# Optimization experiments

Hardware: AMD Instinct MI355X
Metric: run time of the kernel (lower is better)

## Reference

```python
import jax, jax.numpy as jnp
import numpy as np

IMG_C = 256
GC = 32  # graph_channel; must equal graph feature dim 32 for the residual


def setup_inputs() -> dict:
    key = jax.random.key(0)
    ks = jax.random.split(key, 10)
    B, N, WH_SIDE = 8, 4096, 64
    s = lambda fan_in: 1.0 / np.sqrt(fan_in)
    return {
        "input_graph": jax.random.normal(ks[0], (B, N, GC), jnp.float32),
        "input_image": jax.random.normal(ks[1], (B, IMG_C, WH_SIDE, WH_SIDE), jnp.float32),
        # Conv1d(kernel=1) weights stored as [out, in]
        "Wq": jax.random.uniform(ks[2], (GC, 32), jnp.float32, -s(32), s(32)),
        "bq": jax.random.uniform(ks[3], (GC,), jnp.float32, -s(32), s(32)),
        "Wk": jax.random.uniform(ks[4], (GC, IMG_C), jnp.float32, -s(IMG_C), s(IMG_C)),
        "bk": jax.random.uniform(ks[5], (GC,), jnp.float32, -s(IMG_C), s(IMG_C)),
        "Wv": jax.random.uniform(ks[6], (GC, IMG_C), jnp.float32, -s(IMG_C), s(IMG_C)),
        "bv": jax.random.uniform(ks[7], (GC,), jnp.float32, -s(IMG_C), s(IMG_C)),
        "Wc": jax.random.uniform(ks[8], (GC, GC), jnp.float32, -s(GC), s(GC)),
        "bc": jax.random.uniform(ks[9], (GC,), jnp.float32, -s(GC), s(GC)),
    }


def reference(input_graph, input_image, Wq, bq, Wk, bk, Wv, bv, Wc, bc):
    B, C, W, H = input_image.shape
    img = input_image.reshape(B, C, W * H)                      # [B, C, L]
    # 1x1 conv projections == channel matmuls
    K = jnp.einsum('oc,bcl->bol', Wk, img) + bk[None, :, None]  # [B, GC, L]
    V = jnp.einsum('oc,bcl->bol', Wv, img) + bv[None, :, None]  # [B, GC, L]
    # Q: graph [B, N, 32] -> conv over channel dim -> [B, N, GC]
    Q = jnp.einsum('oc,bnc->bno', Wq, input_graph) + bq[None, None, :]
    att = jnp.einsum('bno,bol->bnl', Q, K) / jnp.sqrt(jnp.float32(GC))  # [B, N, L]
    # NOTE: original softmax is over dim=1 (the node/query axis)
    att = jax.nn.softmax(att, axis=1)
    message = jnp.einsum('bol,bnl->bon', V, att)                # [B, GC, N]
    out = input_graph.transpose(0, 2, 1) + (
        jnp.einsum('oc,bcn->bon', Wc, message) + bc[None, :, None]
    )                                                           # [B, GC, N]
    return out.transpose(0, 2, 1)                               # [B, N, GC]
```

## Files before the change

### kernel.cpp

```cpp
#include <hip/hip_runtime.h>

#define BB 8
#define NN 4096
#define LL 4096
#define CC 256

typedef short bf16x8 __attribute__((ext_vector_type(8)));
typedef _Float16 f16x8 __attribute__((ext_vector_type(8)));
typedef __fp16 hf16x2 __attribute__((ext_vector_type(2)));
typedef float f32x4 __attribute__((ext_vector_type(4)));

__device__ __forceinline__ short f2bf(float f) {
  union { float f; unsigned u; } v; v.f = f;
  unsigned r = v.u + 0x7fffu + ((v.u >> 16) & 1u);
  return (short)(r >> 16);
}
__device__ __forceinline__ bf16x8 ld8(const float* __restrict__ fp) {
  float4 a = *(const float4*)fp;
  float4 b = *(const float4*)(fp + 4);
  bf16x8 r;
  r[0] = f2bf(a.x); r[1] = f2bf(a.y); r[2] = f2bf(a.z); r[3] = f2bf(a.w);
  r[4] = f2bf(b.x); r[5] = f2bf(b.y); r[6] = f2bf(b.z); r[7] = f2bf(b.w);
  return r;
}

__global__ __launch_bounds__(256) void ka_proj(
    const float* __restrict__ graph, const float* __restrict__ img,
    const float* __restrict__ Wq, const float* __restrict__ bq,
    const float* __restrict__ Wk, const float* __restrict__ bk,
    const float* __restrict__ Wv, const float* __restrict__ bv,
    short* __restrict__ Qb, short* __restrict__ Kt, _Float16* __restrict__ Vt,
    float* __restrict__ Zbuf)
{
  const int tid = threadIdx.x;
  const int w = tid >> 6, lane = tid & 63, lo = lane & 15, q = lane >> 4;
  const int bid = blockIdx.x;
  if (bid < 512) {
    const int b = bid >> 6;
    if (tid < 64) Zbuf[(size_t)b * LL + ((bid & 63) << 6) + tid] = 0.0f;
    const int lt = ((bid & 63) << 6) + (w << 4);
    f32x4 aK0 = {0,0,0,0}, aK1 = {0,0,0,0}, aV0 = {0,0,0,0}, aV1 = {0,0,0,0};
    const float* ib = img + (size_t)b * CC * LL + lt + lo;
    #pragma unroll
    for (int cs = 0; cs < 8; ++cs) {
      const int c0 = cs * 32 + q * 8;
      bf16x8 bi;
      #pragma unroll
      for (int j = 0; j < 8; ++j) bi[j] = f2bf(ib[(size_t)(c0 + j) * LL]);
      bf16x8 wk0 = ld8(Wk + lo * CC + c0);
      bf16x8 wk1 = ld8(Wk + (lo + 16) * CC + c0);
      bf16x8 wv0 = ld8(Wv + lo * CC + c0);
      bf16x8 wv1 = ld8(Wv + (lo + 16) * CC + c0);
      aK0 = __builtin_amdgcn_mfma_f32_16x16x32_bf16(wk0, bi, aK0, 0, 0, 0);
      aK1 = __builtin_amdgcn_mfma_f32_16x16x32_bf16(wk1, bi, aK1, 0, 0, 0);
      aV0 = __builtin_amdgcn_mfma_f32_16x16x32_bf16(wv0, bi, aV0, 0, 0, 0);
      aV1 = __builtin_amdgcn_mfma_f32_16x16x32_bf16(wv1, bi, aV1, 0, 0, 0);
    }
    const float kscale = 0.2550348663f;
    const size_t row = ((size_t)b * LL + lt + lo) * 32;
    short4 s0, s1;
    s0.x = f2bf((aK0[0] + bk[q * 4 + 0]) * kscale);
    s0.y = f2bf((aK0[1] + bk[q * 4 + 1]) * kscale);
    s0.z = f2bf((aK0[2] + bk[q * 4 + 2]) * kscale);
    s0.w = f2bf((aK0[3] + bk[q * 4 + 3]) * kscale);
    s1.x = f2bf((aK1[0] + bk[16 + q * 4 + 0]) * kscale);
    s1.y = f2bf((aK1[1] + bk[16 + q * 4 + 1]) * kscale);
    s1.z = f2bf((aK1[2] + bk[16 + q * 4 + 2]) * kscale);
    s1.w = f2bf((aK1[3] + bk[16 + q * 4 + 3]) * kscale);
    *(short4*)(Kt + row + q * 4) = s0;
    *(short4*)(Kt + row + 16 + q * 4) = s1;
    union { hf16x2 h[2]; uint2 u; } p0, p1;
    p0.h[0] = __builtin_amdgcn_cvt_pkrtz(aV0[0] + bv[q * 4 + 0], aV0[1] + bv[q * 4 + 1]);
    p0.h[1] = __builtin_amdgcn_cvt_pkrtz(aV0[2] + bv[q * 4 + 2], aV0[3] + bv[q * 4 + 3]);
    p1.h[0] = __builtin_amdgcn_cvt_pkrtz(aV1[0] + bv[16 + q * 4 + 0], aV1[1] + bv[16 + q * 4 + 1]);
    p1.h[1] = __builtin_amdgcn_cvt_pkrtz(aV1[2] + bv[16 + q * 4 + 2], aV1[3] + bv[16 + q * 4 + 3]);
    *(uint2*)(Vt + row + q * 4) = p0.u;
    *(uint2*)(Vt + row + 16 + q * 4) = p1.u;
  } else {
    const int t = bid - 512;
    const int b = t >> 6;
    const int nt = ((t & 63) << 6) + (w << 4);
    bf16x8 ag = ld8(graph + ((size_t)b * NN + nt + lo) * 32 + q * 8);
    bf16x8 w0 = ld8(Wq + lo * 32 + q * 8);
    bf16x8 w1 = ld8(Wq + (lo + 16) * 32 + q * 8);
    f32x4 z = {0,0,0,0};
    f32x4 a0 = __builtin_amdgcn_mfma_f32_16x16x32_bf16(ag, w0, z, 0, 0, 0);
    f32x4 a1 = __builtin_amdgcn_mfma_f32_16x16x32_bf16(ag, w1, z, 0, 0, 0);
    const float b0 = bq[lo], b1 = bq[lo + 16];
    #pragma unroll
    for (int r = 0; r < 4; ++r) {
      const size_t rowq = ((size_t)b * NN + nt + q * 4 + r) * 32;
      Qb[rowq + lo] = f2bf(a0[r] + b0);
      Qb[rowq + 16 + lo] = f2bf(a1[r] + b1);
    }
  }
}

__global__ __launch_bounds__(256) void kb1_z(
    const short* __restrict__ Qb, const short* __restrict__ Kt,
    float* __restrict__ Z)
{
  const int tid = threadIdx.x;
  const int w = tid >> 6, lane = tid & 63, lo = lane & 15, q = lane >> 4;
  const int bid = blockIdx.x;
  const int b = bid >> 8;
  const int l0 = ((bid >> 2) & 63) << 6;
  const int nq = bid & 3;
  bf16x8 kf[4];
  #pragma unroll
  for (int f = 0; f < 4; ++f)
    kf[f] = *(const bf16x8*)(Kt + ((size_t)b * LL + l0 + f * 16 + lo) * 32 + q * 8);
  float za[4][4] = {{0}};
  const short* qbase = Qb + ((size_t)b * NN + nq * 1024 + w * 256 + lo) * 32 + q * 8;
  #pragma unroll 4
  for (int it = 0; it < 16; ++it) {
    bf16x8 qf = *(const bf16x8*)(qbase + it * 512);
    #pragma unroll
    for (int f = 0; f < 4; ++f) {
      f32x4 z = {0,0,0,0};
      f32x4 c = __builtin_amdgcn_mfma_f32_16x16x32_bf16(kf[f], qf, z, 0, 0, 0);
      #pragma unroll
      for (int r = 0; r < 4; ++r) za[f][r] += __builtin_amdgcn_exp2f(c[r]);
    }
  }
  #pragma unroll
  for (int m = 1; m < 16; m <<= 1)
    #pragma unroll
    for (int f = 0; f < 4; ++f)
      #pragma unroll
      for (int r = 0; r < 4; ++r)
        za[f][r] += __shfl_xor(za[f][r], m, 64);
  if (lo == 0) {
    #pragma unroll
    for (int f = 0; f < 4; ++f)
      #pragma unroll
      for (int r = 0; r < 4; ++r)
        atomicAdd(&Z[(size_t)b * LL + l0 + f * 16 + q * 4 + r], za[f][r]);
  }
}

__global__ __launch_bounds__(256) void kb2_scale(
    const _Float16* __restrict__ Vt, const float* __restrict__ Z,
    _Float16* __restrict__ Vpp)
{
  const int tid = threadIdx.x;
  const int b = blockIdx.x >> 6;
  const int l = ((blockIdx.x & 63) << 6) + (tid & 63);
  const int og = tid >> 6;
  const float inv = __builtin_amdgcn_rcpf(Z[(size_t)b * LL + l]) * 4096.0f;
  const f16x8 vv = *(const f16x8*)(Vt + ((size_t)b * LL + l) * 32 + og * 8);
  #pragma unroll
  for (int j = 0; j < 8; ++j)
    Vpp[((size_t)b * 32 + og * 8 + j) * LL + l] = (_Float16)((float)vv[j] * inv);
}

__global__ __launch_bounds__(256) void kc_attn(
    const short* __restrict__ Qb, const short* __restrict__ Kt,
    const _Float16* __restrict__ Vpp, const float* __restrict__ graph,
    const float* __restrict__ Wc, const float* __restrict__ bc,
    float* __restrict__ out)
{
  __shared__ __align__(16) unsigned char smem[4 * 32 * 72 * 2];
  const int tid = threadIdx.x;
  const int w = tid >> 6, lane = tid & 63, lo = lane & 15, q = lane >> 4;
  const int b = blockIdx.x >> 7;
  const int n0 = (blockIdx.x & 127) << 5;
  _Float16* Pw = (_Float16*)smem + w * (32 * 72);
  float* MS = (float*)smem;
  const bf16x8 qf0 = *(const bf16x8*)(Qb + ((size_t)b * NN + n0 + lo) * 32 + q * 8);
  const bf16x8 qf1 = *(const bf16x8*)(Qb + ((size_t)b * NN + n0 + 16 + lo) * 32 + q * 8);
  f32x4 m00 = {0,0,0,0}, m01 = {0,0,0,0}, m10 = {0,0,0,0}, m11 = {0,0,0,0};
  const short* ktb = Kt + (size_t)b * LL * 32 + lo * 32 + q * 8;
  const _Float16* vb0 = Vpp + ((size_t)b * 32 + lo) * LL;
  const _Float16* vb1 = vb0 + (size_t)16 * LL;
  const int lc0 = w * 16;
  bf16x8 kfN[4];
  #pragma unroll
  for (int f = 0; f < 4; ++f)
    kfN[f] = *(const bf16x8*)(ktb + (size_t)(lc0 * 64 + f * 16) * 32);
  for (int lc = lc0; lc < lc0 + 16; ++lc) {
    const int lbase = lc * 64;
    bf16x8 kfC[4];
    #pragma unroll
    for (int f = 0; f < 4; ++f) kfC[f] = kfN[f];
    f16x8 vA0 = *(const f16x8*)(vb0 + lbase + q * 8);
    f16x8 vA1 = *(const f16x8*)(vb0 + lbase + 32 + q * 8);
    f16x8 vB0 = *(const f16x8*)(vb1 + lbase + q * 8);
    f16x8 vB1 = *(const f16x8*)(vb1 + lbase + 32 + q * 8);
    const int lcn = (lc + 1 < lc0 + 16) ? lc + 1 : lc;
    #pragma unroll
    for (int f = 0; f < 4; ++f)
      kfN[f] = *(const bf16x8*)(ktb + (size_t)(lcn * 64 + f * 16) * 32);
    #pragma unroll
    for (int f = 0; f < 4; ++f) {
      f32x4 z = {0,0,0,0};
      f32x4 c0 = __builtin_amdgcn_mfma_f32_16x16x32_bf16(kfC[f], qf0, z, 0, 0, 0);
      f32x4 c1 = __builtin_amdgcn_mfma_f32_16x16x32_bf16(kfC[f], qf1, z, 0, 0, 0);
      union { hf16x2 h[2]; uint2 u; } pk0, pk1;
      pk0.h[0] = __builtin_amdgcn_cvt_pkrtz(__builtin_amdgcn_exp2f(c0[0]),
                                            __builtin_amdgcn_exp2f(c0[1]));
      pk0.h[1] = __builtin_amdgcn_cvt_pkrtz(__builtin_amdgcn_exp2f(c0[2]),
                                            __builtin_amdgcn_exp2f(c0[3]));
      pk1.h[0] = __builtin_amdgcn_cvt_pkrtz(__builtin_amdgcn_exp2f(c1[0]),
                                            __builtin_amdgcn_exp2f(c1[1]));
      pk1.h[1] = __builtin_amdgcn_cvt_pkrtz(__builtin_amdgcn_exp2f(c1[2]),
                                            __builtin_amdgcn_exp2f(c1[3]));
      *(uint2*)&Pw[lo * 72 + f * 16 + q * 4] = pk0.u;
      *(uint2*)&Pw[(16 + lo) * 72 + f * 16 + q * 4] = pk1.u;
    }
    {
      f16x8 pa00 = *(const f16x8*)&Pw[lo * 72 + q * 8];
      f16x8 pa01 = *(const f16x8*)&Pw[lo * 72 + 32 + q * 8];
      f16x8 pa10 = *(const f16x8*)&Pw[(16 + lo) * 72 + q * 8];
      f16x8 pa11 = *(const f16x8*)&Pw[(16 + lo) * 72 + 32 + q * 8];
      m00 = __builtin_amdgcn_mfma_f32_16x16x32_f16(pa00, vA0, m00, 0, 0, 0);
      m10 = __builtin_amdgcn_mfma_f32_16x16x32_f16(pa10, vA0, m10, 0, 0, 0);
      m01 = __builtin_amdgcn_mfma_f32_16x16x32_f16(pa00, vB0, m01, 0, 0, 0);
      m11 = __builtin_amdgcn_mfma_f32_16x16x32_f16(pa10, vB0, m11, 0, 0, 0);
      m00 = __builtin_amdgcn_mfma_f32_16x16x32_f16(pa01, vA1, m00, 0, 0, 0);
      m10 = __builtin_amdgcn_mfma_f32_16x16x32_f16(pa11, vA1, m10, 0, 0, 0);
      m01 = __builtin_amdgcn_mfma_f32_16x16x32_f16(pa01, vB1, m01, 0, 0, 0);
      m11 = __builtin_amdgcn_mfma_f32_16x16x32_f16(pa11, vB1, m11, 0, 0, 0);
    }
  }
  float* MSw = MS + w * (32 * 36);
  #pragma unroll
  for (int r = 0; r < 4; ++r) {
    MSw[(q * 4 + r) * 36 + lo] = m00[r];
    MSw[(q * 4 + r) * 36 + 16 + lo] = m01[r];
    MSw[(16 + q * 4 + r) * 36 + lo] = m10[r];
    MSw[(16 + q * 4 + r) * 36 + 16 + lo] = m11[r];
  }
  __syncthreads();
  const int o = lane & 31, nh = lane >> 5;
  float wcr[32];
  #pragma unroll
  for (int c4 = 0; c4 < 8; ++c4) {
    float4 wc4 = *(const float4*)(Wc + o * 32 + c4 * 4);
    wcr[c4 * 4 + 0] = wc4.x * (1.0f / 4096.0f);
    wcr[c4 * 4 + 1] = wc4.y * (1.0f / 4096.0f);
    wcr[c4 * 4 + 2] = wc4.z * (1.0f / 4096.0f);
    wcr[c4 * 4 + 3] = wc4.w * (1.0f / 4096.0f);
  }
  const float bcv = bc[o];
  #pragma unroll
  for (int rr = 0; rr < 4; ++rr) {
    const int nl = w * 8 + nh * 4 + rr;
    f32x4 s = {0,0,0,0};
    #pragma unroll
    for (int cc = 0; cc < 8; ++cc) {
      f32x4 ma = *(const f32x4*)&MS[0 * 1152 + nl * 36 + cc * 4];
      f32x4 mb = *(const f32x4*)&MS[1 * 1152 + nl * 36 + cc * 4];
      f32x4 mc = *(const f32x4*)&MS[2 * 1152 + nl * 36 + cc * 4];
      f32x4 md = *(const f32x4*)&MS[3 * 1152 + nl * 36 + cc * 4];
      f32x4 m4 = ma + mb + mc + md;
      s[0] += wcr[cc * 4 + 0] * m4[0];
      s[1] += wcr[cc * 4 + 1] * m4[1];
      s[2] += wcr[cc * 4 + 2] * m4[2];
      s[3] += wcr[cc * 4 + 3] * m4[3];
    }
    const size_t idx = ((size_t)b * NN + n0 + nl) * 32 + o;
    out[idx] = s[0] + s[1] + s[2] + s[3] + bcv + graph[idx];
  }
}

extern "C" void kernel_launch(void* const* d_in, const int* in_sizes, int n_in,
                              void* d_out, int out_size, void* d_ws, size_t ws_size,
                              hipStream_t stream) {
  const float* graph = (const float*)d_in[0];
  const float* img   = (const float*)d_in[1];
  const float* Wq    = (const float*)d_in[2];
  const float* bq    = (const float*)d_in[3];
  const float* Wk    = (const float*)d_in[4];
  const float* bk    = (const float*)d_in[5];
  const float* Wv    = (const float*)d_in[6];
  const float* bv    = (const float*)d_in[7];
  const float* Wc    = (const float*)d_in[8];
  const float* bc    = (const float*)d_in[9];
  char* ws = (char*)d_ws;
  short*    Qb  = (short*)(ws + 0);
  short*    Kt  = (short*)(ws + 2097152);
  _Float16* Vt  = (_Float16*)(ws + 4194304);
  _Float16* Vpp = (_Float16*)(ws + 6291456);
  float*    Zb  = (float*)(ws + 8388608);
  ka_proj<<<dim3(1024), dim3(256), 0, stream>>>(graph, img, Wq, bq, Wk, bk, Wv, bv,
                                                Qb, Kt, Vt, Zb);
  kb1_z<<<dim3(2048), dim3(256), 0, stream>>>(Qb, Kt, Zb);
  kb2_scale<<<dim3(512), dim3(256), 0, stream>>>(Vt, Zb, Vpp);
  kc_attn<<<dim3(1024), dim3(256), 0, stream>>>(Qb, Kt, Vpp, graph, Wc, bc,
                                                (float*)d_out);
}
```

Before: 183.1 us.

## Split attention over L into two halves with separate output-projection kernel

The attention kernel now splits the L dimension into two halves, doubling the grid to 2048 blocks. Each block writes its partial message sums to a workspace buffer, and a new kernel adds the two partials and applies the Wc projection, bias and residual. This is meant to give more parallelism and shorter per-block loops, helped by launch bounds that request 8 waves per SIMD. The Z-reduction kernel also replaces unroll-by-4 with explicit one-ahead prefetching of Q fragments. In exchange it adds an extra launch and a round trip of the partial messages through global memory.

```diff
diff --git a/kernel.cpp b/kernel.cpp
--- a/kernel.cpp
+++ b/kernel.cpp
@@ -96,7 +96,7 @@
   }
 }
 
-__global__ __launch_bounds__(256) void kb1_z(
+__global__ __launch_bounds__(256, 8) void kb1_z(
     const short* __restrict__ Qb, const short* __restrict__ Kt,
     float* __restrict__ Z)
 {
@@ -112,9 +112,10 @@
     kf[f] = *(const bf16x8*)(Kt + ((size_t)b * LL + l0 + f * 16 + lo) * 32 + q * 8);
   float za[4][4] = {{0}};
   const short* qbase = Qb + ((size_t)b * NN + nq * 1024 + w * 256 + lo) * 32 + q * 8;
-  #pragma unroll 4
+  bf16x8 qf = *(const bf16x8*)qbase;
   for (int it = 0; it < 16; ++it) {
-    bf16x8 qf = *(const bf16x8*)(qbase + it * 512);
+    const int itn = (it + 1 < 16) ? it + 1 : it;
+    bf16x8 qn = *(const bf16x8*)(qbase + itn * 512);
     #pragma unroll
     for (int f = 0; f < 4; ++f) {
       f32x4 z = {0,0,0,0};
@@ -122,6 +123,7 @@
       #pragma unroll
       for (int r = 0; r < 4; ++r) za[f][r] += __builtin_amdgcn_exp2f(c[r]);
     }
+    qf = qn;
   }
   #pragma unroll
   for (int m = 1; m < 16; m <<= 1)
@@ -154,17 +156,17 @@
     Vpp[((size_t)b * 32 + og * 8 + j) * LL + l] = (_Float16)((float)vv[j] * inv);
 }
 
-__global__ __launch_bounds__(256) void kc_attn(
+__global__ __launch_bounds__(256, 8) void kc1_attn(
     const short* __restrict__ Qb, const short* __restrict__ Kt,
-    const _Float16* __restrict__ Vpp, const float* __restrict__ graph,
-    const float* __restrict__ Wc, const float* __restrict__ bc,
-    float* __restrict__ out)
-{
-  __shared__ __align__(16) unsigned char smem[4 * 32 * 72 * 2];
+    const _Float16* __restrict__ Vpp, float* __restrict__ msgpart)
+{
+  __shared__ __align__(16) unsigned char smem[18432];
   const int tid = threadIdx.x;
   const int w = tid >> 6, lane = tid & 63, lo = lane & 15, q = lane >> 4;
-  const int b = blockIdx.x >> 7;
-  const int n0 = (blockIdx.x & 127) << 5;
+  const int bid = blockIdx.x;
+  const int b = bid >> 8;
+  const int half = (bid >> 7) & 1;
+  const int n0 = (bid & 127) << 5;
   _Float16* Pw = (_Float16*)smem + w * (32 * 72);
   float* MS = (float*)smem;
   const bf16x8 qf0 = *(const bf16x8*)(Qb + ((size_t)b * NN + n0 + lo) * 32 + q * 8);
@@ -173,12 +175,12 @@
   const short* ktb = Kt + (size_t)b * LL * 32 + lo * 32 + q * 8;
   const _Float16* vb0 = Vpp + ((size_t)b * 32 + lo) * LL;
   const _Float16* vb1 = vb0 + (size_t)16 * LL;
-  const int lc0 = w * 16;
+  const int lc0 = half * 32 + w * 8;
   bf16x8 kfN[4];
   #pragma unroll
   for (int f = 0; f < 4; ++f)
     kfN[f] = *(const bf16x8*)(ktb + (size_t)(lc0 * 64 + f * 16) * 32);
-  for (int lc = lc0; lc < lc0 + 16; ++lc) {
+  for (int lc = lc0; lc < lc0 + 8; ++lc) {
     const int lbase = lc * 64;
     bf16x8 kfC[4];
     #pragma unroll
@@ -187,7 +189,7 @@
     f16x8 vA1 = *(const f16x8*)(vb0 + lbase + 32 + q * 8);
     f16x8 vB0 = *(const f16x8*)(vb1 + lbase + q * 8);
     f16x8 vB1 = *(const f16x8*)(vb1 + lbase + 32 + q * 8);
-    const int lcn = (lc + 1 < lc0 + 16) ? lc + 1 : lc;
+    const int lcn = (lc + 1 < lc0 + 8) ? lc + 1 : lc;
     #pragma unroll
     for (int f = 0; f < 4; ++f)
       kfN[f] = *(const bf16x8*)(ktb + (size_t)(lcn * 64 + f * 16) * 32);
@@ -232,35 +234,46 @@
     MSw[(16 + q * 4 + r) * 36 + 16 + lo] = m11[r];
   }
   __syncthreads();
-  const int o = lane & 31, nh = lane >> 5;
-  float wcr[32];
+  const int nl = tid >> 3, oq = (tid & 7) << 2;
+  f32x4 s = *(const f32x4*)&MS[0 * 1152 + nl * 36 + oq];
+  s += *(const f32x4*)&MS[1 * 1152 + nl * 36 + oq];
+  s += *(const f32x4*)&MS[2 * 1152 + nl * 36 + oq];
+  s += *(const f32x4*)&MS[3 * 1152 + nl * 36 + oq];
+  *(f32x4*)(msgpart + (((size_t)half * BB + b) * NN + n0 + nl) * 32 + oq) = s;
+}
+
+__global__ __launch_bounds__(256) void kc2_out(
+    const float* __restrict__ msgpart, const float* __restrict__ graph,
+    const float* __restrict__ Wc, const float* __restrict__ bc,
+    float* __restrict__ out)
+{
+  const int tid = threadIdx.x;
+  const int b = blockIdx.x >> 7;
+  const int n = ((blockIdx.x & 127) << 5) + (tid >> 3);
+  const int oq = (tid & 7) << 2;
+  const float* mp0 = msgpart + ((size_t)b * NN + n) * 32;
+  const float* mp1 = msgpart + ((size_t)(BB + b) * NN + n) * 32;
+  float m[32];
   #pragma unroll
   for (int c4 = 0; c4 < 8; ++c4) {
-    float4 wc4 = *(const float4*)(Wc + o * 32 + c4 * 4);
-    wcr[c4 * 4 + 0] = wc4.x * (1.0f / 4096.0f);
-    wcr[c4 * 4 + 1] = wc4.y * (1.0f / 4096.0f);
-    wcr[c4 * 4 + 2] = wc4.z * (1.0f / 4096.0f);
-    wcr[c4 * 4 + 3] = wc4.w * (1.0f / 4096.0f);
-  }
-  const float bcv = bc[o];
-  #pragma unroll
-  for (int rr = 0; rr < 4; ++rr) {
-    const int nl = w * 8 + nh * 4 + rr;
-    f32x4 s = {0,0,0,0};
-    #pragma unroll
-    for (int cc = 0; cc < 8; ++cc) {
-      f32x4 ma = *(const f32x4*)&MS[0 * 1152 + nl * 36 + cc * 4];
-      f32x4 mb = *(const f32x4*)&MS[1 * 1152 + nl * 36 + cc * 4];
-      f32x4 mc = *(const f32x4*)&MS[2 * 1152 + nl * 36 + cc * 4];
-      f32x4 md = *(const f32x4*)&MS[3 * 1152 + nl * 36 + cc * 4];
-      f32x4 m4 = ma + mb + mc + md;
-      s[0] += wcr[cc * 4 + 0] * m4[0];
-      s[1] += wcr[cc * 4 + 1] * m4[1];
-      s[2] += wcr[cc * 4 + 2] * m4[2];
-      s[3] += wcr[cc * 4 + 3] * m4[3];
-    }
-    const size_t idx = ((size_t)b * NN + n0 + nl) * 32 + o;
-    out[idx] = s[0] + s[1] + s[2] + s[3] + bcv + graph[idx];
+    f32x4 a = *(const f32x4*)(mp0 + c4 * 4);
+    f32x4 bsum = *(const f32x4*)(mp1 + c4 * 4);
+    f32x4 s = a + bsum;
+    m[c4 * 4 + 0] = s[0]; m[c4 * 4 + 1] = s[1];
+    m[c4 * 4 + 2] = s[2]; m[c4 * 4 + 3] = s[3];
+  }
+  #pragma unroll
+  for (int j = 0; j < 4; ++j) {
+    const int o = oq + j;
+    float acc = 0.0f;
+    #pragma unroll
+    for (int c4 = 0; c4 < 8; ++c4) {
+      f32x4 wv = *(const f32x4*)(Wc + o * 32 + c4 * 4);
+      acc += wv[0] * m[c4 * 4 + 0] + wv[1] * m[c4 * 4 + 1]
+           + wv[2] * m[c4 * 4 + 2] + wv[3] * m[c4 * 4 + 3];
+    }
+    const size_t idx = ((size_t)b * NN + n) * 32 + o;
+    out[idx] = acc * (1.0f / 4096.0f) + bc[o] + graph[idx];
   }
 }
 
@@ -283,10 +296,11 @@
   _Float16* Vt  = (_Float16*)(ws + 4194304);
   _Float16* Vpp = (_Float16*)(ws + 6291456);
   float*    Zb  = (float*)(ws + 8388608);
+  float*    Mp  = (float*)(ws + 8519680);
   ka_proj<<<dim3(1024), dim3(256), 0, stream>>>(graph, img, Wq, bq, Wk, bk, Wv, bv,
                                                 Qb, Kt, Vt, Zb);
   kb1_z<<<dim3(2048), dim3(256), 0, stream>>>(Qb, Kt, Zb);
   kb2_scale<<<dim3(512), dim3(256), 0, stream>>>(Vt, Zb, Vpp);
-  kc_attn<<<dim3(1024), dim3(256), 0, stream>>>(Qb, Kt, Vpp, graph, Wc, bc,
-                                                (float*)d_out);
-}
+  kc1_attn<<<dim3(2048), dim3(256), 0, stream>>>(Qb, Kt, Vpp, Mp);
+  kc2_out<<<dim3(1024), dim3(256), 0, stream>>>(Mp, graph, Wc, bc, (float*)d_out);
+}
```

New measurement: 196.0 us. 7.0% more time.
